# Kernel optimization log

Hardware: AMD Instinct MI355X
Metric: run time of the kernel (lower is better)

Reference implementation:

```python
import jax, jax.numpy as jnp
import numpy as np

N_NODES = 50000
N_EDGES = 800000
D_FEAT = 64
HIDDEN = 128
OUT = 16


def sage_conv(x, src, dst, W_l, W_r, b):
    # PyG SAGEConv (aggr='mean', root_weight=True):
    #   out = lin_l(mean_{j in N(i)} x_j) + lin_r(x_i)
    n = x.shape[0]
    msg = x[src]                                        # [E, d] gather
    agg = jax.ops.segment_sum(msg, dst, num_segments=n) # [N, d]
    deg = jax.ops.segment_sum(jnp.ones((src.shape[0],), x.dtype), dst, num_segments=n)
    mean = agg / jnp.maximum(deg, 1.0)[:, None]         # 0 for isolated nodes
    return mean @ W_l + b + x @ W_r


def setup_inputs() -> dict:
    key = jax.random.key(0)
    ks = jax.random.split(key, 8)
    s = lambda d: 1.0 / np.sqrt(d)
    return {
        "x": jax.random.normal(ks[0], (N_NODES, D_FEAT), dtype=jnp.float32),
        "edge_index": jax.random.randint(ks[1], (2, N_EDGES), 0, N_NODES, dtype=jnp.int32),
        "W1_l": jax.random.normal(ks[2], (D_FEAT, HIDDEN), dtype=jnp.float32) * s(D_FEAT),
        "W1_r": jax.random.normal(ks[3], (D_FEAT, HIDDEN), dtype=jnp.float32) * s(D_FEAT),
        "b1": jnp.zeros((HIDDEN,), dtype=jnp.float32),
        "W2_l": jax.random.normal(ks[4], (HIDDEN, OUT), dtype=jnp.float32) * s(HIDDEN),
        "W2_r": jax.random.normal(ks[5], (HIDDEN, OUT), dtype=jnp.float32) * s(HIDDEN),
        "b2": jnp.zeros((OUT,), dtype=jnp.float32),
    }


def reference(x, edge_index, W1_l, W1_r, b1, W2_l, W2_r, b2):
    src, dst = edge_index[0], edge_index[1]
    h = jax.nn.relu(sage_conv(x, src, dst, W1_l, W1_r, b1))
    h = sage_conv(h, src, dst, W2_l, W2_r, b2)
    # eval-mode path of the original module
    return jax.nn.softmax(h, axis=1)
```

## Files before the change

### kernel.cpp

```cpp
#include <hip/hip_runtime.h>
#include <math.h>

#define N_NODES 50000
#define N_EDGES 800000
#define D_FEAT  64
#define HIDDEN  128
#define OUT     16

#define NBUCK   98
#define BUCKB   512
#define NBINA   256
#define EPB     (N_EDGES / NBINA)
#define CCAP    72
#define PBLK    800
#define SEGS    8
#define CPS     (NBINA / SEGS)
#define CAPE    16
#define ASTR    (SEGS * CAPE)

typedef unsigned short ushort_t;
typedef unsigned char uchar_t;
typedef unsigned int uint_t;
typedef __attribute__((ext_vector_type(8))) __bf16 bf16x8;
typedef __attribute__((ext_vector_type(8))) _Float16 half8;
typedef __attribute__((ext_vector_type(4))) float f32x4;

__device__ __forceinline__ void split8(const float* u, bf16x8& ah, bf16x8& al) {
    #pragma unroll
    for (int i = 0; i < 8; ++i) {
        const __bf16 h = (__bf16)u[i];
        ah[i] = h;
        al[i] = (__bf16)(u[i] - (float)h);
    }
}

__global__ __launch_bounds__(256) void binA_kernel(
        const int* __restrict__ ei,
        int* __restrict__ bcntG,
        uint_t* __restrict__ ebuf,
        const float* __restrict__ x,
        const float* __restrict__ W1l, const float* __restrict__ W1r,
        const float* __restrict__ W2l, const float* __restrict__ W2r,
        _Float16* __restrict__ xh,
        __bf16* __restrict__ Whi1, __bf16* __restrict__ Wlo1,
        __bf16* __restrict__ Whi2, __bf16* __restrict__ Wlo2) {
    const int blk = blockIdx.x;
    if (blk < NBINA) {
        __shared__ int lcur[NBUCK];
        for (int i = threadIdx.x; i < NBUCK; i += 256) lcur[i] = 0;
        __syncthreads();
        const int base = blk * EPB;
        for (int i = threadIdx.x; i < EPB; i += 256) {
            const int e = base + i;
            const uint_t s = (uint_t)ei[e];
            const uint_t d = (uint_t)ei[N_EDGES + e];
            const int b = (int)(d >> 9);
            const int r = atomicAdd(&lcur[b], 1);
            if (r < CCAP)
                ebuf[((size_t)b * NBINA + blk) * CCAP + r] = s | (d << 16);
        }
        __syncthreads();
        for (int i = threadIdx.x; i < NBUCK; i += 256) {
            int c = lcur[i];
            if (c > CCAP) c = CCAP;
            bcntG[i * NBINA + blk] = c;
        }
        return;
    }
    const int idx = (blk - NBINA) * 256 + threadIdx.x;
    if (idx < N_NODES * D_FEAT / 16) {
        const float4* xp = (const float4*)(x + idx * 16);
        const float4 a = xp[0], b = xp[1], c = xp[2], d = xp[3];
        half8 h0, h1;
        h0[0] = (_Float16)a.x; h0[1] = (_Float16)a.y; h0[2] = (_Float16)a.z; h0[3] = (_Float16)a.w;
        h0[4] = (_Float16)b.x; h0[5] = (_Float16)b.y; h0[6] = (_Float16)b.z; h0[7] = (_Float16)b.w;
        h1[0] = (_Float16)c.x; h1[1] = (_Float16)c.y; h1[2] = (_Float16)c.z; h1[3] = (_Float16)c.w;
        h1[4] = (_Float16)d.x; h1[5] = (_Float16)d.y; h1[6] = (_Float16)d.z; h1[7] = (_Float16)d.w;
        *(half8*)(xh + idx * 16) = h0;
        *(half8*)(xh + idx * 16 + 8) = h1;
    }
    if (idx < 16384) {
        const int k = idx >> 7, c = idx & 127;
        const float v = (k < 64) ? W1l[k * HIDDEN + c] : W1r[(k - 64) * HIDDEN + c];
        const int kt = k >> 5, gg = (k >> 3) & 3, j = k & 7;
        const int pos = (((kt * 8 + (c >> 4)) * 64) + (gg * 16 + (c & 15))) * 8 + j;
        const __bf16 h = (__bf16)v;
        Whi1[pos] = h;
        Wlo1[pos] = (__bf16)(v - (float)h);
    } else if (idx < 20480) {
        const int i2 = idx - 16384;
        const int k = i2 >> 5, c = i2 & 31;
        const float v = (c < 16) ? W2l[k * OUT + c] : W2r[k * OUT + (c - 16)];
        const int kt = k >> 5, gg = (k >> 3) & 3, j = k & 7;
        const int pos = (((kt * 2 + (c >> 4)) * 64) + (gg * 16 + (c & 15))) * 8 + j;
        const __bf16 h = (__bf16)v;
        Whi2[pos] = h;
        Wlo2[pos] = (__bf16)(v - (float)h);
    }
}

__global__ __launch_bounds__(256) void binB_kernel(
        const uint_t* __restrict__ ebuf,
        const int* __restrict__ bcntG,
        ushort_t* __restrict__ adj,
        uchar_t* __restrict__ cnt8) {
    __shared__ int scnt[BUCKB];
    const int b = blockIdx.x / SEGS;
    const int s = blockIdx.x - b * SEGS;
    const int lo = b << 9;
    for (int i = threadIdx.x; i < BUCKB; i += 256) scnt[i] = 0;
    __syncthreads();
    const int wave = threadIdx.x >> 6, lane = threadIdx.x & 63;
    for (int c = s * CPS + wave; c < s * CPS + CPS; c += 4) {
        const int cc = bcntG[b * NBINA + c];
        const uint_t* eb = ebuf + ((size_t)b * NBINA + c) * CCAP;
        for (int off = lane; off < cc; off += 64) {
            const uint_t u = eb[off];
            const int dl = (int)(u >> 16) - lo;
            const int sl = atomicAdd(&scnt[dl], 1);
            if (sl < CAPE)
                adj[(size_t)(lo + dl) * ASTR + s * CAPE + sl] =
                    (ushort_t)(u & 0xFFFFu);
        }
    }
    __syncthreads();
    for (int i = threadIdx.x; i < BUCKB; i += 256) {
        const int node = lo + i;
        if (node < N_NODES) {
            int c = scnt[i];
            if (c > CAPE) c = CAPE;
            cnt8[(size_t)node * SEGS + s] = (uchar_t)c;
        }
    }
}

__global__ __launch_bounds__(256) void gather_mean_kernel(
        const _Float16* __restrict__ xh,
        const ushort_t* __restrict__ adj,
        const uchar_t* __restrict__ cnt8,
        _Float16* __restrict__ meanh) {
    const int w = (blockIdx.x * 256 + threadIdx.x) >> 6;
    if (w >= N_NODES) return;
    const int lane = threadIdx.x & 63;
    const int eg = lane >> 3, fq = lane & 7;
    const uint2 cu = *(const uint2*)(cnt8 + (size_t)w * SEGS);
    const uint_t cw = (eg < 4) ? cu.x : cu.y;
    const int ce = (cw >> ((eg & 3) * 8)) & 0xFF;
    const int deg = (cu.x & 0xFF) + ((cu.x >> 8) & 0xFF) + ((cu.x >> 16) & 0xFF) + (cu.x >> 24)
                  + (cu.y & 0xFF) + ((cu.y >> 8) & 0xFF) + ((cu.y >> 16) & 0xFF) + (cu.y >> 24);
    const ushort_t* ab = adj + (size_t)w * ASTR + eg * CAPE;
    float acc[8];
    #pragma unroll
    for (int i = 0; i < 8; ++i) acc[i] = 0.f;
    for (int j = 0; j < ce; ++j) {
        const int s = ab[j];
        const half8 v = *(const half8*)(xh + s * D_FEAT + 8 * fq);
        #pragma unroll
        for (int i = 0; i < 8; ++i) acc[i] += (float)v[i];
    }
    #pragma unroll
    for (int off = 32; off >= 8; off >>= 1) {
        #pragma unroll
        for (int i = 0; i < 8; ++i) acc[i] += __shfl_down(acc[i], off);
    }
    if (lane < 8) {
        const float invd = 1.f / fmaxf((float)deg, 1.f);
        half8 o;
        #pragma unroll
        for (int i = 0; i < 8; ++i) o[i] = (_Float16)(acc[i] * invd);
        *(half8*)(meanh + w * D_FEAT + 8 * fq) = o;
    }
}

__global__ __launch_bounds__(256) void mfma1_kernel(
        const _Float16* __restrict__ xh,
        const _Float16* __restrict__ meanh,
        const __bf16* __restrict__ Whi1, const __bf16* __restrict__ Wlo1,
        const __bf16* __restrict__ Whi2, const __bf16* __restrict__ Wlo2,
        const float* __restrict__ b1,
        _Float16* __restrict__ zh, _Float16* __restrict__ rh) {
    __shared__ float Hs[4][16][132];
    const int w = threadIdx.x >> 6;
    const int l = threadIdx.x & 63;
    const int g = l >> 4;
    const int col = l & 15;
    const int nodebase = blockIdx.x * 64 + w * 16;
    const int nA = nodebase + col;

    f32x4 acc[8];
    #pragma unroll
    for (int ct = 0; ct < 8; ++ct) acc[ct] = (f32x4){0.f, 0.f, 0.f, 0.f};

    #pragma unroll
    for (int kt = 0; kt < 4; ++kt) {
        float u[8];
        #pragma unroll
        for (int i = 0; i < 8; ++i) u[i] = 0.f;
        if (nA < N_NODES) {
            const _Float16* src = (kt < 2) ? meanh : xh;
            const half8 hv = *(const half8*)(src + (size_t)nA * 64 + (kt & 1) * 32 + g * 8);
            #pragma unroll
            for (int i = 0; i < 8; ++i) u[i] = (float)hv[i];
        }
        bf16x8 ah, al;
        split8(u, ah, al);
        #pragma unroll
        for (int ct = 0; ct < 8; ++ct) {
            const int fo = ((kt * 8 + ct) * 64 + l) * 8;
            const bf16x8 bh = *(const bf16x8*)(Whi1 + fo);
            const bf16x8 bl = *(const bf16x8*)(Wlo1 + fo);
            acc[ct] = __builtin_amdgcn_mfma_f32_16x16x32_bf16(ah, bh, acc[ct], 0, 0, 0);
            acc[ct] = __builtin_amdgcn_mfma_f32_16x16x32_bf16(al, bh, acc[ct], 0, 0, 0);
            acc[ct] = __builtin_amdgcn_mfma_f32_16x16x32_bf16(ah, bl, acc[ct], 0, 0, 0);
        }
    }

    #pragma unroll
    for (int ct = 0; ct < 8; ++ct) {
        const float bv = b1[ct * 16 + col];
        #pragma unroll
        for (int i = 0; i < 4; ++i)
            Hs[w][g * 4 + i][ct * 16 + col] = fmaxf(acc[ct][i] + bv, 0.f);
    }

    f32x4 acc2[2];
    acc2[0] = (f32x4){0.f, 0.f, 0.f, 0.f};
    acc2[1] = (f32x4){0.f, 0.f, 0.f, 0.f};
    #pragma unroll
    for (int kt2 = 0; kt2 < 4; ++kt2) {
        const float* hp = &Hs[w][col][kt2 * 32 + g * 8];
        const float4 u0 = *(const float4*)hp;
        const float4 u1 = *(const float4*)(hp + 4);
        float u[8];
        u[0] = u0.x; u[1] = u0.y; u[2] = u0.z; u[3] = u0.w;
        u[4] = u1.x; u[5] = u1.y; u[6] = u1.z; u[7] = u1.w;
        bf16x8 ah, al;
        split8(u, ah, al);
        #pragma unroll
        for (int ct2 = 0; ct2 < 2; ++ct2) {
            const int fo = ((kt2 * 2 + ct2) * 64 + l) * 8;
            const bf16x8 bh = *(const bf16x8*)(Whi2 + fo);
            const bf16x8 bl = *(const bf16x8*)(Wlo2 + fo);
            acc2[ct2] = __builtin_amdgcn_mfma_f32_16x16x32_bf16(ah, bh, acc2[ct2], 0, 0, 0);
            acc2[ct2] = __builtin_amdgcn_mfma_f32_16x16x32_bf16(al, bh, acc2[ct2], 0, 0, 0);
            acc2[ct2] = __builtin_amdgcn_mfma_f32_16x16x32_bf16(ah, bl, acc2[ct2], 0, 0, 0);
        }
    }
    #pragma unroll
    for (int ct2 = 0; ct2 < 2; ++ct2) {
        _Float16* dst = ct2 ? rh : zh;
        #pragma unroll
        for (int i = 0; i < 4; ++i) {
            const int node = nodebase + g * 4 + i;
            if (node < N_NODES) dst[node * OUT + col] = (_Float16)acc2[ct2][i];
        }
    }
}

__global__ __launch_bounds__(256) void fused2_kernel(
        const _Float16* __restrict__ zh,
        const _Float16* __restrict__ rh,
        const ushort_t* __restrict__ adj,
        const uchar_t* __restrict__ cnt8,
        const float* __restrict__ b2,
        float* __restrict__ out) {
    const int w = (blockIdx.x * 256 + threadIdx.x) >> 6;
    if (w >= N_NODES) return;
    const int lane = threadIdx.x & 63;
    const int h = lane & 1;
    const int eg = lane >> 1;
    const int seg = eg >> 2, j0 = eg & 3;
    const uint2 cu = *(const uint2*)(cnt8 + (size_t)w * SEGS);
    const uint_t cw = (seg < 4) ? cu.x : cu.y;
    const int ce = (cw >> ((seg & 3) * 8)) & 0xFF;
    const int deg = (cu.x & 0xFF) + ((cu.x >> 8) & 0xFF) + ((cu.x >> 16) & 0xFF) + (cu.x >> 24)
                  + (cu.y & 0xFF) + ((cu.y >> 8) & 0xFF) + ((cu.y >> 16) & 0xFF) + (cu.y >> 24);
    const ushort_t* ab = adj + (size_t)w * ASTR + seg * CAPE;
    float acc[8];
    #pragma unroll
    for (int i = 0; i < 8; ++i) acc[i] = 0.f;
    for (int j = j0; j < ce; j += 4) {
        const half8 v = *(const half8*)(zh + ab[j] * OUT + 8 * h);
        #pragma unroll
        for (int i = 0; i < 8; ++i) acc[i] += (float)v[i];
    }
    #pragma unroll
    for (int off = 32; off >= 2; off >>= 1) {
        #pragma unroll
        for (int i = 0; i < 8; ++i) acc[i] += __shfl_down(acc[i], off);
    }
    const float invd = 1.f / fmaxf((float)deg, 1.f);
    const half8 rv = *(const half8*)(rh + (size_t)w * OUT + 8 * h);
    float v[8];
    #pragma unroll
    for (int i = 0; i < 8; ++i)
        v[i] = acc[i] * invd + (float)rv[i] + b2[8 * h + i];
    float m = v[0];
    #pragma unroll
    for (int i = 1; i < 8; ++i) m = fmaxf(m, v[i]);
    m = fmaxf(m, __shfl_xor(m, 1));
    float e[8], t = 0.f;
    #pragma unroll
    for (int i = 0; i < 8; ++i) { e[i] = __expf(v[i] - m); t += e[i]; }
    t += __shfl_xor(t, 1);
    if (lane < 2) {
        const float it = 1.f / t;
        float4 o0, o1;
        o0.x = e[0] * it; o0.y = e[1] * it; o0.z = e[2] * it; o0.w = e[3] * it;
        o1.x = e[4] * it; o1.y = e[5] * it; o1.z = e[6] * it; o1.w = e[7] * it;
        float4* op = (float4*)(out + (size_t)w * OUT + 8 * h);
        op[0] = o0;
        op[1] = o1;
    }
}

extern "C" void kernel_launch(void* const* d_in, const int* in_sizes, int n_in,
                              void* d_out, int out_size, void* d_ws, size_t ws_size,
                              hipStream_t stream) {
    const float* x   = (const float*)d_in[0];
    const int*   ei  = (const int*)d_in[1];
    const float* W1l = (const float*)d_in[2];
    const float* W1r = (const float*)d_in[3];
    const float* b1  = (const float*)d_in[4];
    const float* W2l = (const float*)d_in[5];
    const float* W2r = (const float*)d_in[6];
    const float* b2  = (const float*)d_in[7];
    float* out = (float*)d_out;

    char* wsB = (char*)d_ws;
    int*       bcntG = (int*)wsB;
    uint_t*    ebuf  = (uint_t*)(wsB + 102400);
    _Float16*  meanh = (_Float16*)(wsB + 102400);
    ushort_t*  adj   = (ushort_t*)(wsB + 7327744);
    uchar_t*   cnt8  = (uchar_t*)(wsB + 20127744);
    _Float16*  xh    = (_Float16*)(wsB + 20527744);
    _Float16*  zh    = (_Float16*)(wsB + 26927744);
    _Float16*  rh    = (_Float16*)(wsB + 28527744);
    __bf16*    Whi1  = (__bf16*)(wsB + 30127744);
    __bf16*    Wlo1  = Whi1 + 16384;
    __bf16*    Whi2  = Wlo1 + 16384;
    __bf16*    Wlo2  = Whi2 + 4096;

    binA_kernel<<<NBINA + PBLK, 256, 0, stream>>>(ei, bcntG, ebuf, x,
                                                  W1l, W1r, W2l, W2r,
                                                  xh, Whi1, Wlo1, Whi2, Wlo2);
    binB_kernel<<<NBUCK * SEGS, 256, 0, stream>>>(ebuf, bcntG, adj, cnt8);
    gather_mean_kernel<<<N_NODES / 4, 256, 0, stream>>>(xh, adj, cnt8, meanh);
    mfma1_kernel<<<(N_NODES + 63) / 64, 256, 0, stream>>>(
        xh, meanh, Whi1, Wlo1, Whi2, Wlo2, b1, zh, rh);
    fused2_kernel<<<N_NODES / 4, 256, 0, stream>>>(zh, rh, adj, cnt8, b2, out);
}
```

Baseline: 101.1 us.

## Fuse neighbor mean gather into layer-1 MFMA kernel via shared memory

Merges the gather-mean kernel into the first MFMA kernel. Each 64-node tile computes its neighbor means into an LDS buffer, and the MFMA stage reads them from there. This removes one kernel launch and the round trip of the mean array through global memory. In exchange, grid parallelism for the gather phase drops from 12500 blocks to 782, and each wave now processes 16 nodes sequentially, which may reduce latency hiding for the random gathers.

```diff
diff --git a/kernel.cpp b/kernel.cpp
--- a/kernel.cpp
+++ b/kernel.cpp
@@ -134,57 +134,62 @@
     }
 }
 
-__global__ __launch_bounds__(256) void gather_mean_kernel(
+__global__ __launch_bounds__(256) void fused1_kernel(
         const _Float16* __restrict__ xh,
         const ushort_t* __restrict__ adj,
         const uchar_t* __restrict__ cnt8,
-        _Float16* __restrict__ meanh) {
-    const int w = (blockIdx.x * 256 + threadIdx.x) >> 6;
-    if (w >= N_NODES) return;
-    const int lane = threadIdx.x & 63;
-    const int eg = lane >> 3, fq = lane & 7;
-    const uint2 cu = *(const uint2*)(cnt8 + (size_t)w * SEGS);
-    const uint_t cw = (eg < 4) ? cu.x : cu.y;
-    const int ce = (cw >> ((eg & 3) * 8)) & 0xFF;
-    const int deg = (cu.x & 0xFF) + ((cu.x >> 8) & 0xFF) + ((cu.x >> 16) & 0xFF) + (cu.x >> 24)
-                  + (cu.y & 0xFF) + ((cu.y >> 8) & 0xFF) + ((cu.y >> 16) & 0xFF) + (cu.y >> 24);
-    const ushort_t* ab = adj + (size_t)w * ASTR + eg * CAPE;
-    float acc[8];
-    #pragma unroll
-    for (int i = 0; i < 8; ++i) acc[i] = 0.f;
-    for (int j = 0; j < ce; ++j) {
-        const int s = ab[j];
-        const half8 v = *(const half8*)(xh + s * D_FEAT + 8 * fq);
-        #pragma unroll
-        for (int i = 0; i < 8; ++i) acc[i] += (float)v[i];
-    }
-    #pragma unroll
-    for (int off = 32; off >= 8; off >>= 1) {
-        #pragma unroll
-        for (int i = 0; i < 8; ++i) acc[i] += __shfl_down(acc[i], off);
-    }
-    if (lane < 8) {
-        const float invd = 1.f / fmaxf((float)deg, 1.f);
-        half8 o;
-        #pragma unroll
-        for (int i = 0; i < 8; ++i) o[i] = (_Float16)(acc[i] * invd);
-        *(half8*)(meanh + w * D_FEAT + 8 * fq) = o;
-    }
-}
-
-__global__ __launch_bounds__(256) void mfma1_kernel(
-        const _Float16* __restrict__ xh,
-        const _Float16* __restrict__ meanh,
         const __bf16* __restrict__ Whi1, const __bf16* __restrict__ Wlo1,
         const __bf16* __restrict__ Whi2, const __bf16* __restrict__ Wlo2,
         const float* __restrict__ b1,
         _Float16* __restrict__ zh, _Float16* __restrict__ rh) {
+    __shared__ _Float16 meanL[64][68];
     __shared__ float Hs[4][16][132];
-    const int w = threadIdx.x >> 6;
+    const int wv = threadIdx.x >> 6;
     const int l = threadIdx.x & 63;
+    const int tile = blockIdx.x * 64;
+
+    {
+        const int eg = l >> 3, fq = l & 7;
+        #pragma unroll 2
+        for (int it = 0; it < 16; ++it) {
+            const int nl = wv * 16 + it;
+            const int node = tile + nl;
+            float acc[8];
+            #pragma unroll
+            for (int i = 0; i < 8; ++i) acc[i] = 0.f;
+            int deg = 0;
+            if (node < N_NODES) {
+                const uint2 cu = *(const uint2*)(cnt8 + (size_t)node * SEGS);
+                const uint_t cw = (eg < 4) ? cu.x : cu.y;
+                const int ce = (cw >> ((eg & 3) * 8)) & 0xFF;
+                deg = (cu.x & 0xFF) + ((cu.x >> 8) & 0xFF) + ((cu.x >> 16) & 0xFF) + (cu.x >> 24)
+                    + (cu.y & 0xFF) + ((cu.y >> 8) & 0xFF) + ((cu.y >> 16) & 0xFF) + (cu.y >> 24);
+                const ushort_t* ab = adj + (size_t)node * ASTR + eg * CAPE;
+                for (int j = 0; j < ce; ++j) {
+                    const int s = ab[j];
+                    const half8 v = *(const half8*)(xh + s * D_FEAT + 8 * fq);
+                    #pragma unroll
+                    for (int i = 0; i < 8; ++i) acc[i] += (float)v[i];
+                }
+            }
+            #pragma unroll
+            for (int off = 32; off >= 8; off >>= 1) {
+                #pragma unroll
+                for (int i = 0; i < 8; ++i) acc[i] += __shfl_down(acc[i], off);
+            }
+            if (l < 8) {
+                const float invd = 1.f / fmaxf((float)deg, 1.f);
+                half8 o;
+                #pragma unroll
+                for (int i = 0; i < 8; ++i) o[i] = (_Float16)(acc[i] * invd);
+                *(half8*)&meanL[nl][8 * fq] = o;
+            }
+        }
+    }
+
     const int g = l >> 4;
     const int col = l & 15;
-    const int nodebase = blockIdx.x * 64 + w * 16;
+    const int nodebase = tile + wv * 16;
     const int nA = nodebase + col;
 
     f32x4 acc[8];
@@ -196,9 +201,12 @@
         float u[8];
         #pragma unroll
         for (int i = 0; i < 8; ++i) u[i] = 0.f;
-        if (nA < N_NODES) {
-            const _Float16* src = (kt < 2) ? meanh : xh;
-            const half8 hv = *(const half8*)(src + (size_t)nA * 64 + (kt & 1) * 32 + g * 8);
+        if (kt < 2) {
+            const half8 hv = *(const half8*)&meanL[wv * 16 + col][kt * 32 + g * 8];
+            #pragma unroll
+            for (int i = 0; i < 8; ++i) u[i] = (float)hv[i];
+        } else if (nA < N_NODES) {
+            const half8 hv = *(const half8*)(xh + (size_t)nA * 64 + (kt & 1) * 32 + g * 8);
             #pragma unroll
             for (int i = 0; i < 8; ++i) u[i] = (float)hv[i];
         }
@@ -220,7 +228,7 @@
         const float bv = b1[ct * 16 + col];
         #pragma unroll
         for (int i = 0; i < 4; ++i)
-            Hs[w][g * 4 + i][ct * 16 + col] = fmaxf(acc[ct][i] + bv, 0.f);
+            Hs[wv][g * 4 + i][ct * 16 + col] = fmaxf(acc[ct][i] + bv, 0.f);
     }
 
     f32x4 acc2[2];
@@ -228,7 +236,7 @@
     acc2[1] = (f32x4){0.f, 0.f, 0.f, 0.f};
     #pragma unroll
     for (int kt2 = 0; kt2 < 4; ++kt2) {
-        const float* hp = &Hs[w][col][kt2 * 32 + g * 8];
+        const float* hp = &Hs[wv][col][kt2 * 32 + g * 8];
         const float4 u0 = *(const float4*)hp;
         const float4 u1 = *(const float4*)(hp + 4);
         float u[8];
@@ -330,7 +338,6 @@
     char* wsB = (char*)d_ws;
     int*       bcntG = (int*)wsB;
     uint_t*    ebuf  = (uint_t*)(wsB + 102400);
-    _Float16*  meanh = (_Float16*)(wsB + 102400);
     ushort_t*  adj   = (ushort_t*)(wsB + 7327744);
     uchar_t*   cnt8  = (uchar_t*)(wsB + 20127744);
     _Float16*  xh    = (_Float16*)(wsB + 20527744);
@@ -345,8 +352,7 @@
                                                   W1l, W1r, W2l, W2r,
                                                   xh, Whi1, Wlo1, Whi2, Wlo2);
     binB_kernel<<<NBUCK * SEGS, 256, 0, stream>>>(ebuf, bcntG, adj, cnt8);
-    gather_mean_kernel<<<N_NODES / 4, 256, 0, stream>>>(xh, adj, cnt8, meanh);
-    mfma1_kernel<<<(N_NODES + 63) / 64, 256, 0, stream>>>(
-        xh, meanh, Whi1, Wlo1, Whi2, Wlo2, b1, zh, rh);
+    fused1_kernel<<<(N_NODES + 63) / 64, 256, 0, stream>>>(
+        xh, adj, cnt8, Whi1, Wlo1, Whi2, Wlo2, b1, zh, rh);
     fused2_kernel<<<N_NODES / 4, 256, 0, stream>>>(zh, rh, adj, cnt8, b2, out);
 }
```

Result: slower. 155.8 us (+54.2%).
